# Kernel optimization log

Measured on AMD Instinct MI355X. Metric: run time of the kernel, lower is better.

Reference implementation:

```python
import jax, jax.numpy as jnp
import numpy as np

L1_PENALTY = 0.01
RHO = 5.0
N_ITERS = 100  # fixed iteration count standing in for max_iter=2000 w/ tol
EPS = 1e-12


def _normalize(x):
    # matches torch.nn.functional.normalize(dim=1, eps=1e-12)
    n = jnp.linalg.norm(x, axis=-1, keepdims=True)
    return x / jnp.maximum(n, EPS)


def _admm_nnlasso(D, Y, lam, rho, n_iters):
    """Batched nonnegative Lasso via ADMM.
    Solves per-row: min_w 0.5*||D^T w - y||^2 + lam*||w||_1, w >= 0.
    D: [c, d] dictionary, Y: [B, d] targets. Returns W: [B, c].
    x-update uses Woodbury: (A^T A + rho I)^{-1} b = (b - A^T (G + rho I)^{-1} A b)/rho
    with A = D^T, G = A A^T = D^T D ([d, d], d=512 -> cheap Cholesky).
    """
    d = D.shape[1]
    G = D.T @ D + rho * jnp.eye(d, dtype=D.dtype)  # [d, d]
    cf = jax.scipy.linalg.cho_factor(G)
    Aty = Y @ D.T  # [B, c] = A^T y batched
    thr = lam / rho

    def step(carry, _):
        z, u = carry
        b = Aty + rho * (z - u)               # [B, c]
        s = jax.scipy.linalg.cho_solve(cf, (b @ D).T).T  # [B, d]
        x = (b - s @ D.T) / rho               # [B, c]
        z_new = jnp.maximum(x + u - thr, 0.0)  # nonneg soft-threshold
        u_new = u + x - z_new
        return (z_new, u_new), None

    z0 = jnp.zeros_like(Aty)
    (z, _), _ = jax.lax.scan(step, (z0, z0), None, length=n_iters)
    return z


def setup_inputs() -> dict:
    key = jax.random.key(0)
    k1, k2, k3, k4 = jax.random.split(key, 4)
    B, C, Dm = 1024, 10000, 512
    image = jax.random.normal(k1, (B, Dm), dtype=jnp.float32)
    text = jax.random.normal(k2, (B, Dm), dtype=jnp.float32)
    image_mean = 0.1 * jax.random.normal(k3, (Dm,), dtype=jnp.float32)
    dictionary = jax.random.normal(k4, (C, Dm), dtype=jnp.float32)
    dictionary = dictionary / jnp.linalg.norm(dictionary, axis=1, keepdims=True)
    return {"image": image, "text": text, "image_mean": image_mean,
            "dictionary": dictionary}


def reference(image, text, image_mean, dictionary):
    # encode_image
    img = _normalize(image)
    centered = _normalize(img - image_mean)
    weights = _admm_nnlasso(dictionary, centered, L1_PENALTY, RHO, N_ITERS)
    recon = weights @ dictionary           # [B, d]
    recon = _normalize(recon)
    recon = _normalize(recon + image_mean)
    # encode_text (decomp_text=False -> just normalize)
    txt = _normalize(text)
    return recon, txt
```

## Files before the change

kernel.cpp:

```cpp
#include <hip/hip_runtime.h>
#include <cstddef>
#include <cstdint>

#define BDIM  1024
#define DM    512
#define CREAL 10000
#define CP    10112
#define KSPL  16
#define RHOC  5.0f
#define THRC  (0.01f/5.0f)
#define NIT   100
#define NSIT  12

typedef float f32x4 __attribute__((ext_vector_type(4)));
typedef _Float16 f16x8 __attribute__((ext_vector_type(8)));
typedef _Float16 f16x4 __attribute__((ext_vector_type(4)));
typedef unsigned int u32x4 __attribute__((ext_vector_type(4)));


__device__ __forceinline__ f16x8 scl6(f16x8 v) {
    f16x8 r;
#pragma unroll
    for (int i = 0; i < 8; i++) r[i] = v[i] * (_Float16)0.015625f;
    return r;
}

__device__ __forceinline__ void absfold(f16x8& h8, f16x8& l8) {
    u32x4 h = __builtin_bit_cast(u32x4, h8);
    u32x4 l = __builtin_bit_cast(u32x4, l8);
    u32x4 m = h & 0x80008000u;
    h8 = __builtin_bit_cast(f16x8, h ^ m);
    l8 = __builtin_bit_cast(f16x8, l ^ m);
}

__device__ __forceinline__ void relufold(f16x8& h8, f16x8& l8) {
#pragma unroll
    for (int e = 0; e < 8; e++) {
        bool p = h8[e] > (_Float16)0;
        if (!p) { h8[e] = (_Float16)0; l8[e] = (_Float16)0; }
    }
}

__device__ __forceinline__ size_t psidx(int row, int col) {
    return ((size_t)(row >> 4) * (CP >> 5) + (size_t)(col >> 5)) * 512
         + (size_t)((((col >> 3) & 3) * 16 + (row & 15)) * 8 + (col & 7));
}

__device__ __forceinline__ void dma16(const _Float16* g, _Float16* l) {
    __builtin_amdgcn_global_load_lds(
        (const __attribute__((address_space(1))) void*)g,
        (__attribute__((address_space(3))) void*)l, 16, 0, 0);
}

__device__ __forceinline__ float blk_sum256(float v) {
    __shared__ float sb[4];
#pragma unroll
    for (int o = 32; o; o >>= 1) v += __shfl_down(v, o, 64);
    int lane = threadIdx.x & 63, w = threadIdx.x >> 6;
    __syncthreads();
    if (lane == 0) sb[w] = v;
    __syncthreads();
    return sb[0] + sb[1] + sb[2] + sb[3];
}

__global__ __launch_bounds__(256) void knorm_rows(const float* __restrict__ X,
                                                  float* __restrict__ out) {
    int row = blockIdx.x, t = threadIdx.x;
    int off = row * DM + t * 2;
    float2 v = *(const float2*)(X + off);
    float ss = blk_sum256(v.x * v.x + v.y * v.y);
    float inv = 1.0f / fmaxf(sqrtf(ss), 1e-12f);
    float2 o = {v.x * inv, v.y * inv};
    *(float2*)(out + off) = o;
}

__global__ __launch_bounds__(256) void kprep_Y(const float* __restrict__ img,
                                               const float* __restrict__ mean,
                                               float* __restrict__ Y) {
    int row = blockIdx.x, t = threadIdx.x;
    int off = row * DM + t * 2;
    float2 v = *(const float2*)(img + off);
    float ss = blk_sum256(v.x * v.x + v.y * v.y);
    float inv = 1.0f / fmaxf(sqrtf(ss), 1e-12f);
    float2 mm = *(const float2*)(mean + t * 2);
    float tx = v.x * inv - mm.x, ty = v.y * inv - mm.y;
    float ss2 = blk_sum256(tx * tx + ty * ty);
    float inv2 = 1.0f / fmaxf(sqrtf(ss2), 1e-12f);
    float2 o = {tx * inv2, ty * inv2};
    *(float2*)(Y + off) = o;
}

__global__ __launch_bounds__(256) void ktrs(const float* __restrict__ in,
                                            float* __restrict__ out32,
                                            _Float16* __restrict__ oH,
                                            _Float16* __restrict__ oL,
                                            int Rvalid, int Cin, int Rout) {
    __shared__ float tile[64][65];
    int r0 = blockIdx.x * 64;
    int c0 = blockIdx.y * 64;
    int t = threadIdx.x;
    int ri = r0 + (t >> 2);
    int cc = (t & 3) * 16;
#pragma unroll
    for (int q = 0; q < 4; ++q) {
        float4 v = {0.f, 0.f, 0.f, 0.f};
        if (ri < Rvalid) v = *(const float4*)(in + (size_t)ri * Cin + c0 + cc + q * 4);
        *(float4*)&tile[t >> 2][cc + q * 4] = v;
    }
    __syncthreads();
    int oc = c0 + (t >> 2);
    int orr = r0 + (t & 3) * 16;
    _Float16 hv[16], lv[16];
#pragma unroll
    for (int q = 0; q < 16; ++q) {
        float v = tile[(t & 3) * 16 + q][t >> 2];
        _Float16 h = (_Float16)v;
        _Float16 l = (_Float16)((v - (float)h) * 64.f);
        hv[q] = h; lv[q] = l;
        if (out32) out32[(size_t)oc * Rout + orr + q] = (float)h + (float)l * 0.015625f;
    }
    int rt = oc >> 4, rin = oc & 15;
    int kt = orr >> 5;
    int kq0 = (orr >> 3) & 3;
    size_t base = ((size_t)rt * (Rout >> 5) + kt) * 512;
    *(f16x8*)(oH + base + (size_t)(kq0 * 16 + rin) * 8)       = *(f16x8*)&hv[0];
    *(f16x8*)(oH + base + (size_t)((kq0 + 1) * 16 + rin) * 8) = *(f16x8*)&hv[8];
    *(f16x8*)(oL + base + (size_t)(kq0 * 16 + rin) * 8)       = *(f16x8*)&lv[0];
    *(f16x8*)(oL + base + (size_t)((kq0 + 1) * 16 + rin) * 8) = *(f16x8*)&lv[8];
}

__global__ void kcsum(const float* __restrict__ Dt, float* __restrict__ csum) {
    int n = blockIdx.x, t = threadIdx.x;
    float s = 0.f;
    for (int k = t; k < CP; k += 64) s += Dt[(size_t)n * CP + k];
#pragma unroll
    for (int o = 32; o; o >>= 1) s += __shfl_down(s, o, 64);
    if (t == 0) csum[n] = s;
}

__global__ __launch_bounds__(256) void kG(const float* __restrict__ Dt,
                                          float* __restrict__ G) {
    __shared__ float As[32][68];
    __shared__ float Bs[32][68];
    int tid = threadIdx.x;
    int j0 = blockIdx.x * 64, i0 = blockIdx.y * 64;
    int tn = (tid & 15) * 4, tm = (tid >> 4) * 4;
    float acc[4][4];
#pragma unroll
    for (int i = 0; i < 4; i++)
#pragma unroll
        for (int j = 0; j < 4; j++) acc[i][j] = 0.f;
    for (int k0 = 0; k0 < CP; k0 += 32) {
        __syncthreads();
#pragma unroll
        for (int p = 0; p < 2; ++p) {
            int idx = tid + p * 256;
            int row = idx >> 3, kv = (idx & 7) << 2;
            float4 va = *(const float4*)(Dt + (size_t)(i0 + row) * CP + k0 + kv);
            As[kv + 0][row] = va.x; As[kv + 1][row] = va.y;
            As[kv + 2][row] = va.z; As[kv + 3][row] = va.w;
            float4 vb = *(const float4*)(Dt + (size_t)(j0 + row) * CP + k0 + kv);
            Bs[kv + 0][row] = vb.x; Bs[kv + 1][row] = vb.y;
            Bs[kv + 2][row] = vb.z; Bs[kv + 3][row] = vb.w;
        }
        __syncthreads();
#pragma unroll
        for (int k = 0; k < 32; ++k) {
            float4 a4 = *(const float4*)&As[k][tm];
            float4 b4 = *(const float4*)&Bs[k][tn];
            float af[4] = {a4.x, a4.y, a4.z, a4.w};
            float bf[4] = {b4.x, b4.y, b4.z, b4.w};
#pragma unroll
            for (int i = 0; i < 4; i++)
#pragma unroll
                for (int j = 0; j < 4; j++) acc[i][j] = fmaf(af[i], bf[j], acc[i][j]);
        }
    }
#pragma unroll
    for (int i = 0; i < 4; i++)
#pragma unroll
        for (int j = 0; j < 4; j++) {
            int gi = i0 + tm + i, gj = j0 + tn + j;
            G[gi * DM + gj] = acc[i][j] + ((gi == gj) ? RHOC : 0.f);
        }
}

__global__ void krow_abssum(const float* __restrict__ G, float* __restrict__ gmax) {
    int row = blockIdx.x, t = threadIdx.x;
    float s = 0.f;
    for (int j = t; j < DM; j += 64) s += fabsf(G[row * DM + j]);
#pragma unroll
    for (int o = 32; o; o >>= 1) s += __shfl_down(s, o, 64);
    if (t == 0) atomicMax((int*)gmax, __float_as_int(s));
}

__global__ void kinit_X0(const float* __restrict__ gmax, float* __restrict__ X) {
    int idx = blockIdx.x * 256 + threadIdx.x;
    int i = idx >> 9, j = idx & 511;
    X[idx] = (i == j) ? (1.0f / gmax[0]) : 0.0f;
}

__global__ __launch_bounds__(256) void kgemm_ns_T(const float* __restrict__ G,
                                                  const float* __restrict__ X,
                                                  float* __restrict__ T) {
    __shared__ float As[32][68];
    __shared__ float Bs[32][68];
    int tid = threadIdx.x;
    int n0 = blockIdx.x * 64, m0 = blockIdx.y * 64;
    int tn = (tid & 15) * 4, tm = (tid >> 4) * 4;
    float acc[4][4];
#pragma unroll
    for (int i = 0; i < 4; i++)
#pragma unroll
        for (int j = 0; j < 4; j++) acc[i][j] = 0.f;
    for (int k0 = 0; k0 < DM; k0 += 32) {
        __syncthreads();
#pragma unroll
        for (int p = 0; p < 2; ++p) {
            int idx = tid + p * 256;
            {
                int row = idx >> 3, kv = (idx & 7) << 2;
                float4 v = *(const float4*)(G + (m0 + row) * DM + k0 + kv);
                As[kv + 0][row] = v.x; As[kv + 1][row] = v.y;
                As[kv + 2][row] = v.z; As[kv + 3][row] = v.w;
            }
            {
                int r = idx >> 4, cv = (idx & 15) << 2;
                *(float4*)&Bs[r][cv] = *(const float4*)(X + (k0 + r) * DM + n0 + cv);
            }
        }
        __syncthreads();
#pragma unroll
        for (int k = 0; k < 32; ++k) {
            float4 a4 = *(const float4*)&As[k][tm];
            float4 b4 = *(const float4*)&Bs[k][tn];
            float af[4] = {a4.x, a4.y, a4.z, a4.w};
            float bf[4] = {b4.x, b4.y, b4.z, b4.w};
#pragma unroll
            for (int i = 0; i < 4; i++)
#pragma unroll
                for (int j = 0; j < 4; j++) acc[i][j] = fmaf(af[i], bf[j], acc[i][j]);
        }
    }
#pragma unroll
    for (int i = 0; i < 4; i++) {
        float4 o = {acc[i][0], acc[i][1], acc[i][2], acc[i][3]};
        *(float4*)(T + (m0 + tm + i) * DM + n0 + tn) = o;
    }
}

__global__ __launch_bounds__(256) void kgemm_ns_X(const float* __restrict__ Xo,
                                                  const float* __restrict__ T,
                                                  float* __restrict__ Xn) {
    __shared__ float As[32][68];
    __shared__ float Bs[32][68];
    int tid = threadIdx.x;
    int n0 = blockIdx.x * 64, m0 = blockIdx.y * 64;
    int tn = (tid & 15) * 4, tm = (tid >> 4) * 4;
    float acc[4][4];
#pragma unroll
    for (int i = 0; i < 4; i++)
#pragma unroll
        for (int j = 0; j < 4; j++) acc[i][j] = 0.f;
    for (int k0 = 0; k0 < DM; k0 += 32) {
        __syncthreads();
#pragma unroll
        for (int p = 0; p < 2; ++p) {
            int idx = tid + p * 256;
            {
                int row = idx >> 3, kv = (idx & 7) << 2;
                float4 v = *(const float4*)(Xo + (m0 + row) * DM + k0 + kv);
                As[kv + 0][row] = v.x; As[kv + 1][row] = v.y;
                As[kv + 2][row] = v.z; As[kv + 3][row] = v.w;
            }
            {
                int r = idx >> 4, cv = (idx & 15) << 2;
                *(float4*)&Bs[r][cv] = *(const float4*)(T + (k0 + r) * DM + n0 + cv);
            }
        }
        __syncthreads();
#pragma unroll
        for (int k = 0; k < 32; ++k) {
            float4 a4 = *(const float4*)&As[k][tm];
            float4 b4 = *(const float4*)&Bs[k][tn];
            float af[4] = {a4.x, a4.y, a4.z, a4.w};
            float bf[4] = {b4.x, b4.y, b4.z, b4.w};
#pragma unroll
            for (int i = 0; i < 4; i++)
#pragma unroll
                for (int j = 0; j < 4; j++) acc[i][j] = fmaf(af[i], bf[j], acc[i][j]);
        }
    }
#pragma unroll
    for (int i = 0; i < 4; i++) {
        int base = (m0 + tm + i) * DM + n0 + tn;
        float4 xo = *(const float4*)(Xo + base);
        float4 o = {2.f * xo.x - acc[i][0], 2.f * xo.y - acc[i][1],
                    2.f * xo.z - acc[i][2], 2.f * xo.w - acc[i][3]};
        *(float4*)(Xn + base) = o;
    }
}

template <int MODE>
__global__ __launch_bounds__(256) void kgemm_nn64(const float* __restrict__ A,
                                                  const float* __restrict__ B,
                                                  float* __restrict__ out32,
                                                  _Float16* __restrict__ oA) {
    __shared__ float As[32][68];
    __shared__ float Bs[32][68];
    int tid = threadIdx.x;
    int n0 = blockIdx.x * 64, m0 = blockIdx.y * 64;
    int tn = (tid & 15) * 4, tm = (tid >> 4) * 4;
    float acc[4][4];
#pragma unroll
    for (int i = 0; i < 4; i++)
#pragma unroll
        for (int j = 0; j < 4; j++) acc[i][j] = 0.f;
    for (int k0 = 0; k0 < DM; k0 += 32) {
        __syncthreads();
#pragma unroll
        for (int p = 0; p < 2; ++p) {
            int idx = tid + p * 256;
            {
                int row = idx >> 3, kv = (idx & 7) << 2;
                float4 v = *(const float4*)(A + (size_t)(m0 + row) * DM + k0 + kv);
                As[kv + 0][row] = v.x; As[kv + 1][row] = v.y;
                As[kv + 2][row] = v.z; As[kv + 3][row] = v.w;
            }
            {
                int r = idx >> 4, cv = (idx & 15) << 2;
                *(float4*)&Bs[r][cv] = *(const float4*)(B + (size_t)(k0 + r) * CP + n0 + cv);
            }
        }
        __syncthreads();
#pragma unroll
        for (int k = 0; k < 32; ++k) {
            float4 a4 = *(const float4*)&As[k][tm];
            float4 b4 = *(const float4*)&Bs[k][tn];
            float af[4] = {a4.x, a4.y, a4.z, a4.w};
            float bf[4] = {b4.x, b4.y, b4.z, b4.w};
#pragma unroll
            for (int i = 0; i < 4; i++)
#pragma unroll
                for (int j = 0; j < 4; j++) acc[i][j] = fmaf(af[i], bf[j], acc[i][j]);
        }
    }
#pragma unroll
    for (int i = 0; i < 4; i++)
#pragma unroll
        for (int j = 0; j < 4; j++) {
            int row = m0 + tm + i, col = n0 + tn + j;
            if (MODE == 0) out32[(size_t)row * CP + col] = acc[i][j];
            else           oA[psidx(row, col)] = (_Float16)(acc[i][j] * 0.2f * 64.f);
        }
}

__global__ __launch_bounds__(256) void kgemm_aD(const float* __restrict__ Yb,
                                                const float* __restrict__ G,
                                                const float* __restrict__ csum,
                                                float* __restrict__ aD) {
    __shared__ float As[32][68];
    __shared__ float Bs[32][68];
    int tid = threadIdx.x;
    int n0 = blockIdx.x * 64, m0 = blockIdx.y * 64;
    int tn = (tid & 15) * 4, tm = (tid >> 4) * 4;
    float acc[4][4];
#pragma unroll
    for (int i = 0; i < 4; i++)
#pragma unroll
        for (int j = 0; j < 4; j++) acc[i][j] = 0.f;
    for (int k0 = 0; k0 < DM; k0 += 32) {
        __syncthreads();
#pragma unroll
        for (int p = 0; p < 2; ++p) {
            int idx = tid + p * 256;
            {
                int row = idx >> 3, kv = (idx & 7) << 2;
                float4 v = *(const float4*)(Yb + (size_t)(m0 + row) * DM + k0 + kv);
                As[kv + 0][row] = v.x; As[kv + 1][row] = v.y;
                As[kv + 2][row] = v.z; As[kv + 3][row] = v.w;
            }
            {
                int r = idx >> 4, cv = (idx & 15) << 2;
                *(float4*)&Bs[r][cv] = *(const float4*)(G + (k0 + r) * DM + n0 + cv);
            }
        }
        __syncthreads();
#pragma unroll
        for (int k = 0; k < 32; ++k) {
            float4 a4 = *(const float4*)&As[k][tm];
            float4 b4 = *(const float4*)&Bs[k][tn];
            float af[4] = {a4.x, a4.y, a4.z, a4.w};
            float bf[4] = {b4.x, b4.y, b4.z, b4.w};
#pragma unroll
            for (int i = 0; i < 4; i++)
#pragma unroll
                for (int j = 0; j < 4; j++) acc[i][j] = fmaf(af[i], bf[j], acc[i][j]);
        }
    }
    float4 c4 = *(const float4*)(csum + n0 + tn);
#pragma unroll
    for (int i = 0; i < 4; i++) {
        int base = (m0 + tm + i) * DM + n0 + tn;
        float4 y4 = *(const float4*)(Yb + base);
        float4 o = {acc[i][0] * 0.2f - y4.x - THRC * c4.x,
                    acc[i][1] * 0.2f - y4.y - THRC * c4.y,
                    acc[i][2] * 0.2f - y4.z - THRC * c4.z,
                    acc[i][3] * 0.2f - y4.w - THRC * c4.w};
        *(float4*)(aD + base) = o;
    }
}

__global__ void kinit_s(_Float16* __restrict__ SHp, _Float16* __restrict__ SLp) {
    size_t i = ((size_t)blockIdx.x * 256 + threadIdx.x) * 8;
    _Float16 h = (_Float16)(-THRC);
    _Float16 l = (_Float16)((-THRC - (float)h) * 64.f);
    f16x8 hv, lv;
#pragma unroll
    for (int e = 0; e < 8; e++) { hv[e] = h; lv[e] = l; }
    *(f16x8*)(SHp + i) = hv;
    *(f16x8*)(SLp + i) = lv;
}


__device__ __forceinline__ void stage2(_Float16* __restrict__ sab,
                                       const _Float16* __restrict__ AHp,
                                       const _Float16* __restrict__ ALp,
                                       const _Float16* __restrict__ BHp,
                                       const _Float16* __restrict__ BLp,
                                       int sp, int mtbB, int ntbB, int ktA, int ktB,
                                       int wvu, int lane) {
#pragma unroll
    for (int k = 0; k < 4; ++k) {
        const int c = wvu * 4 + k;
        const int t = (c >> 1) & 7;
        const int p = c & 1;
        const _Float16* gp;
        if (c < 16) gp = (p ? ALp : AHp) + ((size_t)(mtbB + t) * ktA + sp) * 512 + (size_t)lane * 8;
        else        gp = (p ? BLp : BHp) + ((size_t)(ntbB + t) * ktB + sp) * 512 + (size_t)lane * 8;
        dma16(gp, sab + (size_t)c * 512);
    }
}

template <int FOLD>
__device__ __forceinline__ void compute8(const _Float16* __restrict__ sab,
                                         int wm, int wn, int lane,
                                         f32x4 (&acc)[4][2]) {
    const int ta = wm >> 4;
    const int tb = wn >> 4;
    f16x8 bh[2], bl[2], bs_[2];
#pragma unroll
    for (int j = 0; j < 2; ++j) {
        const _Float16* p = sab + 8192 + (size_t)(tb + j) * 1024 + (size_t)lane * 8;
        bh[j] = *(const f16x8*)p;
        bl[j] = *(const f16x8*)(p + 512);
        bs_[j] = scl6(bh[j]);
    }
    f16x8 ah[4], al[4], as_[4];
#pragma unroll
    for (int i = 0; i < 4; ++i) {
        const _Float16* p = sab + (size_t)(ta + i) * 1024 + (size_t)lane * 8;
        ah[i] = *(const f16x8*)p;
        al[i] = *(const f16x8*)(p + 512);
    }
#pragma unroll
    for (int i = 0; i < 4; ++i) {
        if (FOLD == 0) absfold(ah[i], al[i]);
        else if (FOLD == 1) relufold(ah[i], al[i]);
        as_[i] = scl6(ah[i]);
    }
    __builtin_amdgcn_s_setprio(1);
#pragma unroll
    for (int i = 0; i < 4; ++i)
#pragma unroll
        for (int j = 0; j < 2; ++j) {
            acc[i][j] = __builtin_amdgcn_mfma_f32_16x16x32_f16(ah[i],  bh[j], acc[i][j], 0, 0, 0);
            acc[i][j] = __builtin_amdgcn_mfma_f32_16x16x32_f16(as_[i], bl[j], acc[i][j], 0, 0, 0);
            acc[i][j] = __builtin_amdgcn_mfma_f32_16x16x32_f16(al[i],  bs_[j], acc[i][j], 0, 0, 0);
        }
    __builtin_amdgcn_s_setprio(0);
}

template <int MODE>
__global__ __launch_bounds__(512, 4) void kg1f(const _Float16* __restrict__ SHp,
                                               const _Float16* __restrict__ SLp,
                                               const _Float16* __restrict__ DHs,
                                               const _Float16* __restrict__ DLs,
                                               float* __restrict__ Qp) {
    __shared__ _Float16 sAB[2][16384];
    const int raw = blockIdx.x;
    const int xcd = raw & 7;
    const int r   = raw >> 3;
    const int ks  = xcd * 2 + (r & 1);
    const int q   = r >> 1;
    const int mb  = q >> 2, nb = q & 3;
    const int n0 = nb * 128, m0 = mb * 128;
    const int tid = threadIdx.x;
    const int lane = tid & 63;
    const int wvu = tid >> 6;
    const int wm = (wvu >> 2) * 64;
    const int wn = (wvu & 3) * 32;
    f32x4 acc[4][2] = {};

    const int steps = CP / 32;
    const int per = (steps + KSPL - 1) / KSPL;
    int s0 = ks * per;
    int s1 = s0 + per; if (s1 > steps) s1 = steps;

    const int mtbB = m0 >> 4;
    const int ntbB = n0 >> 4;
    const int KT = CP / 32;

    stage2(sAB[0], SHp, SLp, DHs, DLs, s0, mtbB, ntbB, KT, KT, wvu, lane);
    __syncthreads();

    for (int sp = s0; sp < s1; sp += 2) {
        stage2(sAB[1], SHp, SLp, DHs, DLs, sp + 1, mtbB, ntbB, KT, KT, wvu, lane);
        compute8<MODE>(sAB[0], wm, wn, lane, acc);
        __syncthreads();
        if (sp + 2 < s1)
            stage2(sAB[0], SHp, SLp, DHs, DLs, sp + 2, mtbB, ntbB, KT, KT, wvu, lane);
        compute8<MODE>(sAB[1], wm, wn, lane, acc);
        __syncthreads();
    }

    float* outp = Qp + (size_t)ks * (BDIM * DM);
    const int r0 = (lane >> 4) * 4, c0l = lane & 15;
#pragma unroll
    for (int i = 0; i < 4; i++)
#pragma unroll
        for (int v = 0; v < 4; v++) {
            int row = m0 + wm + i * 16 + r0 + v;
#pragma unroll
            for (int j = 0; j < 2; j++)
                outp[(size_t)row * DM + n0 + wn + j * 16 + c0l] = acc[i][j][v];
        }
}

template <int ADD>
__global__ void kredf(const float* __restrict__ Qp, const float* __restrict__ aD,
                      float* __restrict__ out32, _Float16* __restrict__ QH,
                      _Float16* __restrict__ QL) {
    size_t b = ((size_t)blockIdx.x * 256 + threadIdx.x) * 4;
    float4 s = {0.f, 0.f, 0.f, 0.f};
    if (ADD) s = *(const float4*)(aD + b);
#pragma unroll
    for (int qq = 0; qq < KSPL; qq++) {
        float4 t = *(const float4*)(Qp + (size_t)qq * (BDIM * DM) + b);
        s.x += t.x; s.y += t.y; s.z += t.z; s.w += t.w;
    }
    if (ADD) {
        int row = (int)(b >> 9), col = (int)(b & 511);
        size_t t0 = ((size_t)(row >> 4) * 16 + (size_t)(col >> 5)) * 512
                  + (size_t)((((col >> 3) & 3) * 16 + (row & 15)) * 8 + (col & 7));
        float sv[4] = {s.x, s.y, s.z, s.w};
        f16x4 h4, l4;
#pragma unroll
        for (int e = 0; e < 4; e++) {
            _Float16 h = (_Float16)sv[e];
            h4[e] = h;
            l4[e] = (_Float16)((sv[e] - (float)h) * 64.f);
        }
        *(f16x4*)(QH + t0) = h4;
        *(f16x4*)(QL + t0) = l4;
    } else {
        *(float4*)(out32 + b) = s;
    }
}

__global__ __launch_bounds__(512, 4) void kg2f(const _Float16* __restrict__ QH,
                                               const _Float16* __restrict__ QL,
                                               const _Float16* __restrict__ EHs,
                                               const _Float16* __restrict__ ELs,
                                               const _Float16* __restrict__ AH,
                                               _Float16* __restrict__ SHp,
                                               _Float16* __restrict__ SLp) {
    __shared__ _Float16 sAB[2][16384];
    const int raw = blockIdx.x;
    const int g = raw & 7;
    const int q = raw >> 3;
    const int mb = q & 7, jj = q >> 3;
    const int nb = g * 10 + jj;
    if (nb >= 79) return;
    const int n0 = nb * 128, m0 = mb * 128;
    const int tid = threadIdx.x;
    const int lane = tid & 63;
    const int wvu = tid >> 6;
    const int wm = (wvu >> 2) * 64;
    const int wn = (wvu & 3) * 32;
    const int mtbB = m0 >> 4;
    const int ntbB = n0 >> 4;
    const int KT = DM / 32;
    f32x4 acc[4][2] = {};

    stage2(sAB[0], QH, QL, EHs, ELs, 0, mtbB, ntbB, KT, KT, wvu, lane);
    __syncthreads();

    for (int kk = 0; kk < KT; kk += 2) {
        stage2(sAB[1], QH, QL, EHs, ELs, kk + 1, mtbB, ntbB, KT, KT, wvu, lane);
        compute8<2>(sAB[0], wm, wn, lane, acc);
        __syncthreads();
        if (kk + 2 < KT)
            stage2(sAB[0], QH, QL, EHs, ELs, kk + 2, mtbB, ntbB, KT, KT, wvu, lane);
        compute8<2>(sAB[1], wm, wn, lane, acc);
        __syncthreads();
    }

    const int r0 = (lane >> 4) * 4, c0l = lane & 15;
    const int mtbA = (m0 + wm) >> 4;
    const int ktb  = (n0 + wn) >> 5;
#pragma unroll
    for (int i = 0; i < 4; ++i) {
        float* sT = (float*)(&sAB[i & 1][0]) + wvu * (16 * 36);
#pragma unroll
        for (int j = 0; j < 2; ++j)
#pragma unroll
            for (int v = 0; v < 4; ++v)
                sT[(r0 + v) * 36 + j * 16 + c0l] = acc[i][j][v];
        float e[8];
        *(float4*)&e[0] = *(const float4*)&sT[(lane & 15) * 36 + (lane >> 4) * 8];
        *(float4*)&e[4] = *(const float4*)&sT[(lane & 15) * 36 + (lane >> 4) * 8 + 4];
        size_t base = ((size_t)(mtbA + i) * (CP >> 5) + ktb) * 512 + (size_t)lane * 8;
        f16x8 ah8 = *(const f16x8*)(AH + base);
        f16x8 sh8 = *(const f16x8*)(SHp + base);
        f16x8 sl8 = *(const f16x8*)(SLp + base);
        f16x8 nh, nl;
#pragma unroll
        for (int e8 = 0; e8 < 8; ++e8) {
            float a = (float)ah8[e8] * 0.015625f;
            float sold = (float)sh8[e8] + (float)sl8[e8] * 0.015625f;
            float z = fmaxf(sold, 0.f);
            float pn = a + z - e[e8];
            float sn = pn - THRC;
            _Float16 h = (_Float16)sn;
            nh[e8] = h;
            nl[e8] = (_Float16)((sn - (float)h) * 64.f);
        }
        *(f16x8*)(SHp + base) = nh;
        *(f16x8*)(SLp + base) = nl;
    }
}

__global__ __launch_bounds__(256) void kfinal(const float* __restrict__ Qf,
                                              const float* __restrict__ mean,
                                              float* __restrict__ out) {
    int row = blockIdx.x, t = threadIdx.x;
    int off = row * DM + t * 2;
    float2 qv = *(const float2*)(Qf + off);
    float rx = qv.x, ry = qv.y;
    float ss = blk_sum256(rx * rx + ry * ry);
    float inv = 1.0f / fmaxf(sqrtf(ss), 1e-12f);
    rx *= inv; ry *= inv;
    float2 mm = *(const float2*)(mean + t * 2);
    rx += mm.x; ry += mm.y;
    float ss2 = blk_sum256(rx * rx + ry * ry);
    float inv2 = 1.0f / fmaxf(sqrtf(ss2), 1e-12f);
    float2 o = {rx * inv2, ry * inv2};
    *(float2*)(out + off) = o;
}

extern "C" void kernel_launch(void* const* d_in, const int* in_sizes, int n_in,
                              void* d_out, int out_size, void* d_ws, size_t ws_size,
                              hipStream_t stream) {
    const float* image = (const float*)d_in[0];
    const float* text  = (const float*)d_in[1];
    const float* mean  = (const float*)d_in[2];
    const float* D     = (const float*)d_in[3];
    float* out = (float*)d_out;
    float* ws = (float*)d_ws;

    const size_t PLH = (size_t)DM * CP;
    float* aD   = ws;
    _Float16* QH = (_Float16*)(ws + 524288);
    _Float16* QL = QH + (size_t)BDIM * DM;
    _Float16* DHs = (_Float16*)(ws + 1048576);
    _Float16* DLs = DHs + PLH;
    _Float16* EHs = DLs + PLH;
    _Float16* ELs = EHs + PLH;
    _Float16* AH  = ELs + PLH;
    _Float16* SH  = AH + (size_t)BDIM * CP;
    _Float16* SL  = SH + (size_t)BDIM * CP;
    float* Qp   = (float*)(SL + (size_t)BDIM * CP);
    float* csum = Qp + (size_t)KSPL * BDIM * DM;
    float* gmax = csum + 512;
    float* Dt32 = (float*)SH;
    float* G    = Dt32 + (size_t)DM * CP;
    float* Xa   = G + 262144;
    float* Xb   = Xa + 262144;
    float* Tns  = Xb + 262144;
    float* Y    = Tns + 262144;
    float* Et32 = (float*)AH;

    knorm_rows<<<BDIM, 256, 0, stream>>>(text, out + (size_t)BDIM * DM);
    kprep_Y<<<BDIM, 256, 0, stream>>>(image, mean, Y);
    ktrs<<<dim3(CP / 64, DM / 64), 256, 0, stream>>>(D, Dt32, DHs, DLs, CREAL, DM, CP);
    kcsum<<<DM, 64, 0, stream>>>(Dt32, csum);
    kG<<<dim3(8, 8), 256, 0, stream>>>(Dt32, G);
    (void)hipMemsetAsync(gmax, 0, 4, stream);
    krow_abssum<<<DM, 64, 0, stream>>>(G, gmax);
    kinit_X0<<<DM * DM / 256, 256, 0, stream>>>(gmax, Xa);
    float* xc = Xa;
    float* xn = Xb;
    for (int it = 0; it < NSIT; ++it) {
        kgemm_ns_T<<<dim3(8, 8), 256, 0, stream>>>(G, xc, Tns);
        kgemm_ns_X<<<dim3(8, 8), 256, 0, stream>>>(xc, Tns, xn);
        float* tmp = xc; xc = xn; xn = tmp;
    }
    float* Ginv = xc;
    kgemm_nn64<0><<<dim3(CP / 64, DM / 64), 256, 0, stream>>>(Ginv, Dt32, Et32, nullptr);
    ktrs<<<dim3(DM / 64, CP / 64), 256, 0, stream>>>(Et32, nullptr, EHs, ELs, DM, CP, DM);
    kgemm_nn64<1><<<dim3(CP / 64, BDIM / 64), 256, 0, stream>>>(Y, Dt32, nullptr, AH);
    kgemm_aD<<<dim3(DM / 64, BDIM / 64), 256, 0, stream>>>(Y, G, csum, aD);
    kinit_s<<<(int)((size_t)BDIM * CP / 8 / 256), 256, 0, stream>>>(SH, SL);

    for (int it = 0; it < NIT; ++it) {
        kg1f<0><<<512, 512, 0, stream>>>(SH, SL, DHs, DLs, Qp);
        kredf<1><<<BDIM * DM / 1024, 256, 0, stream>>>(Qp, aD, nullptr, QH, QL);
        kg2f<<<640, 512, 0, stream>>>(QH, QL, EHs, ELs, AH, SH, SL);
    }

    kg1f<1><<<512, 512, 0, stream>>>(SH, SL, DHs, DLs, Qp);
    kredf<0><<<BDIM * DM / 1024, 256, 0, stream>>>(Qp, nullptr, aD, nullptr, nullptr);
    kfinal<<<BDIM, 256, 0, stream>>>(aD, mean, out);
}
```

Measured before the change: 9.524 ms.

## Retile kg2f to 64x128 blocks with 4 waves and dedicated staging

The second ADMM GEMM kernel now uses 64-row by 128-column output tiles with 256 threads (4 waves, each covering 64x32) instead of 128x128 tiles with 512 threads. It gets its own staging and compute helpers, and the grid doubles to 1280 blocks with an XCD-aware mapping. The aim is more blocks, better load balance across CUs and less LDS per block. In exchange, the E operand is reloaded more often because each block covers fewer rows.

```diff
diff --git a/kernel.cpp b/kernel.cpp
--- a/kernel.cpp
+++ b/kernel.cpp
@@ -568,46 +568,98 @@
     }
 }
 
-__global__ __launch_bounds__(512, 4) void kg2f(const _Float16* __restrict__ QH,
+__device__ __forceinline__ void stage_g2(_Float16* __restrict__ sab,
+                                         const _Float16* __restrict__ QHp,
+                                         const _Float16* __restrict__ QLp,
+                                         const _Float16* __restrict__ EHp,
+                                         const _Float16* __restrict__ ELp,
+                                         int sp, int mtbB, int ntbB,
+                                         int wvu, int lane) {
+#pragma unroll
+    for (int k = 0; k < 6; ++k) {
+        const int c = wvu * 6 + k;
+        const _Float16* gp;
+        if (c < 8) {
+            const int t = c >> 1, p = c & 1;
+            gp = (p ? QLp : QHp) + ((size_t)(mtbB + t) * 16 + sp) * 512 + (size_t)lane * 8;
+        } else {
+            const int cc = c - 8, t = cc >> 1, p = cc & 1;
+            gp = (p ? ELp : EHp) + ((size_t)(ntbB + t) * 16 + sp) * 512 + (size_t)lane * 8;
+        }
+        dma16(gp, sab + (size_t)c * 512);
+    }
+}
+
+__device__ __forceinline__ void compute4(const _Float16* __restrict__ sab,
+                                         int wn, int lane, f32x4 (&acc)[4][2]) {
+    const int tb = wn >> 4;
+    f16x8 bh[2], bl[2], bs_[2];
+#pragma unroll
+    for (int j = 0; j < 2; ++j) {
+        const _Float16* p = sab + 4096 + (size_t)(tb + j) * 1024 + (size_t)lane * 8;
+        bh[j] = *(const f16x8*)p;
+        bl[j] = *(const f16x8*)(p + 512);
+        bs_[j] = scl6(bh[j]);
+    }
+    f16x8 ah[4], al[4], as_[4];
+#pragma unroll
+    for (int i = 0; i < 4; ++i) {
+        const _Float16* p = sab + (size_t)i * 1024 + (size_t)lane * 8;
+        ah[i] = *(const f16x8*)p;
+        al[i] = *(const f16x8*)(p + 512);
+        as_[i] = scl6(ah[i]);
+    }
+    __builtin_amdgcn_s_setprio(1);
+#pragma unroll
+    for (int i = 0; i < 4; ++i)
+#pragma unroll
+        for (int j = 0; j < 2; ++j) {
+            acc[i][j] = __builtin_amdgcn_mfma_f32_16x16x32_f16(ah[i],  bh[j], acc[i][j], 0, 0, 0);
+            acc[i][j] = __builtin_amdgcn_mfma_f32_16x16x32_f16(as_[i], bl[j], acc[i][j], 0, 0, 0);
+            acc[i][j] = __builtin_amdgcn_mfma_f32_16x16x32_f16(al[i],  bs_[j], acc[i][j], 0, 0, 0);
+        }
+    __builtin_amdgcn_s_setprio(0);
+}
+
+__global__ __launch_bounds__(256, 3) void kg2f(const _Float16* __restrict__ QH,
                                                const _Float16* __restrict__ QL,
                                                const _Float16* __restrict__ EHs,
                                                const _Float16* __restrict__ ELs,
                                                const _Float16* __restrict__ AH,
                                                _Float16* __restrict__ SHp,
                                                _Float16* __restrict__ SLp) {
-    __shared__ _Float16 sAB[2][16384];
+    __shared__ _Float16 sAB[2][12288];
     const int raw = blockIdx.x;
-    const int g = raw & 7;
-    const int q = raw >> 3;
-    const int mb = q & 7, jj = q >> 3;
-    const int nb = g * 10 + jj;
+    const int xcd = raw & 7;
+    const int r = raw >> 3;
+    const int nb = xcd * 10 + (r >> 4);
+    const int mb = r & 15;
     if (nb >= 79) return;
-    const int n0 = nb * 128, m0 = mb * 128;
+    const int n0 = nb * 128, m0 = mb * 64;
     const int tid = threadIdx.x;
     const int lane = tid & 63;
     const int wvu = tid >> 6;
-    const int wm = (wvu >> 2) * 64;
-    const int wn = (wvu & 3) * 32;
+    const int wn = wvu * 32;
     const int mtbB = m0 >> 4;
     const int ntbB = n0 >> 4;
     const int KT = DM / 32;
     f32x4 acc[4][2] = {};
 
-    stage2(sAB[0], QH, QL, EHs, ELs, 0, mtbB, ntbB, KT, KT, wvu, lane);
+    stage_g2(sAB[0], QH, QL, EHs, ELs, 0, mtbB, ntbB, wvu, lane);
     __syncthreads();
 
     for (int kk = 0; kk < KT; kk += 2) {
-        stage2(sAB[1], QH, QL, EHs, ELs, kk + 1, mtbB, ntbB, KT, KT, wvu, lane);
-        compute8<2>(sAB[0], wm, wn, lane, acc);
+        stage_g2(sAB[1], QH, QL, EHs, ELs, kk + 1, mtbB, ntbB, wvu, lane);
+        compute4(sAB[0], wn, lane, acc);
         __syncthreads();
         if (kk + 2 < KT)
-            stage2(sAB[0], QH, QL, EHs, ELs, kk + 2, mtbB, ntbB, KT, KT, wvu, lane);
-        compute8<2>(sAB[1], wm, wn, lane, acc);
+            stage_g2(sAB[0], QH, QL, EHs, ELs, kk + 2, mtbB, ntbB, wvu, lane);
+        compute4(sAB[1], wn, lane, acc);
         __syncthreads();
     }
 
     const int r0 = (lane >> 4) * 4, c0l = lane & 15;
-    const int mtbA = (m0 + wm) >> 4;
+    const int mtbA = m0 >> 4;
     const int ktb  = (n0 + wn) >> 5;
 #pragma unroll
     for (int i = 0; i < 4; ++i) {
@@ -716,7 +768,7 @@
     for (int it = 0; it < NIT; ++it) {
         kg1f<0><<<512, 512, 0, stream>>>(SH, SL, DHs, DLs, Qp);
         kredf<1><<<BDIM * DM / 1024, 256, 0, stream>>>(Qp, aD, nullptr, QH, QL);
-        kg2f<<<640, 512, 0, stream>>>(QH, QL, EHs, ELs, AH, SH, SL);
+        kg2f<<<8 * 160, 256, 0, stream>>>(QH, QL, EHs, ELs, AH, SH, SL);
     }
 
     kg1f<1><<<512, 512, 0, stream>>>(SH, SL, DHs, DLs, Qp);
```

New measurement: 9.788 ms. +2.8%, slower.

## Fuse split-K reduction into kg1f via per-tile atomic counter barrier

Applied to the files above, without the earlier changes.

The separate split-K reduction kernel is removed from the ADMM loop. Each kg1f block now signals a per-output-tile atomic counter, spins until all 16 K-split blocks of that tile have written their partials, then reduces its slice of rows, adds aD, and writes the hi/lo fp16 split. This saves one kernel launch and a full pass over the partial buffer per iteration. In exchange it relies on all blocks of a tile being co-resident (512 blocks at 4 per CU) to avoid deadlock, uses spin-waiting, and writes scalar rather than vectorised fp16 stores.

```diff
diff --git a/kernel.cpp b/kernel.cpp
--- a/kernel.cpp
+++ b/kernel.cpp
@@ -481,12 +481,17 @@
     __builtin_amdgcn_s_setprio(0);
 }
 
-template <int MODE>
+template <int MODE, int FUSE>
 __global__ __launch_bounds__(512, 4) void kg1f(const _Float16* __restrict__ SHp,
                                                const _Float16* __restrict__ SLp,
                                                const _Float16* __restrict__ DHs,
                                                const _Float16* __restrict__ DLs,
-                                               float* __restrict__ Qp) {
+                                               float* __restrict__ Qp,
+                                               const float* __restrict__ aD,
+                                               _Float16* __restrict__ QH,
+                                               _Float16* __restrict__ QL,
+                                               unsigned* __restrict__ cnt,
+                                               unsigned target) {
     __shared__ _Float16 sAB[2][16384];
     const int raw = blockIdx.x;
     const int xcd = raw & 7;
@@ -535,37 +540,50 @@
             for (int j = 0; j < 2; j++)
                 outp[(size_t)row * DM + n0 + wn + j * 16 + c0l] = acc[i][j][v];
         }
-}
-
-template <int ADD>
-__global__ void kredf(const float* __restrict__ Qp, const float* __restrict__ aD,
-                      float* __restrict__ out32, _Float16* __restrict__ QH,
-                      _Float16* __restrict__ QL) {
+
+    if (FUSE) {
+        __threadfence();
+        __syncthreads();
+        const int tileId = mb * 4 + nb;
+        if (tid == 0) {
+            atomicAdd(&cnt[tileId], 1u);
+            while (atomicAdd(&cnt[tileId], 0u) < target) { }
+        }
+        __syncthreads();
+        __threadfence();
+        const int lr = tid >> 6;
+        const int lc = (tid & 63) * 2;
+        const int grow = m0 + ks * 8 + lr;
+        const int gcol = n0 + lc;
+        size_t off = (size_t)grow * DM + gcol;
+        float2 s2 = *(const float2*)(aD + off);
+#pragma unroll
+        for (int qq = 0; qq < KSPL; qq++) {
+            float2 t2 = *(const float2*)(Qp + (size_t)qq * (BDIM * DM) + off);
+            s2.x += t2.x; s2.y += t2.y;
+        }
+#pragma unroll
+        for (int e = 0; e < 2; e++) {
+            float sv = e ? s2.y : s2.x;
+            int col = gcol + e;
+            size_t t0 = ((size_t)(grow >> 4) * 16 + (size_t)(col >> 5)) * 512
+                      + (size_t)((((col >> 3) & 3) * 16 + (grow & 15)) * 8 + (col & 7));
+            _Float16 h = (_Float16)sv;
+            QH[t0] = h;
+            QL[t0] = (_Float16)((sv - (float)h) * 64.f);
+        }
+    }
+}
+
+__global__ void kredf0(const float* __restrict__ Qp, float* __restrict__ out32) {
     size_t b = ((size_t)blockIdx.x * 256 + threadIdx.x) * 4;
     float4 s = {0.f, 0.f, 0.f, 0.f};
-    if (ADD) s = *(const float4*)(aD + b);
 #pragma unroll
     for (int qq = 0; qq < KSPL; qq++) {
         float4 t = *(const float4*)(Qp + (size_t)qq * (BDIM * DM) + b);
         s.x += t.x; s.y += t.y; s.z += t.z; s.w += t.w;
     }
-    if (ADD) {
-        int row = (int)(b >> 9), col = (int)(b & 511);
-        size_t t0 = ((size_t)(row >> 4) * 16 + (size_t)(col >> 5)) * 512
-                  + (size_t)((((col >> 3) & 3) * 16 + (row & 15)) * 8 + (col & 7));
-        float sv[4] = {s.x, s.y, s.z, s.w};
-        f16x4 h4, l4;
-#pragma unroll
-        for (int e = 0; e < 4; e++) {
-            _Float16 h = (_Float16)sv[e];
-            h4[e] = h;
-            l4[e] = (_Float16)((sv[e] - (float)h) * 64.f);
-        }
-        *(f16x4*)(QH + t0) = h4;
-        *(f16x4*)(QL + t0) = l4;
-    } else {
-        *(float4*)(out32 + b) = s;
-    }
+    *(float4*)(out32 + b) = s;
 }
 
 __global__ __launch_bounds__(512, 4) void kg2f(const _Float16* __restrict__ QH,
@@ -683,6 +701,7 @@
     float* Qp   = (float*)(SL + (size_t)BDIM * CP);
     float* csum = Qp + (size_t)KSPL * BDIM * DM;
     float* gmax = csum + 512;
+    unsigned* cnt = (unsigned*)(gmax + 64);
     float* Dt32 = (float*)SH;
     float* G    = Dt32 + (size_t)DM * CP;
     float* Xa   = G + 262144;
@@ -697,6 +716,7 @@
     kcsum<<<DM, 64, 0, stream>>>(Dt32, csum);
     kG<<<dim3(8, 8), 256, 0, stream>>>(Dt32, G);
     (void)hipMemsetAsync(gmax, 0, 4, stream);
+    (void)hipMemsetAsync(cnt, 0, 32 * sizeof(unsigned), stream);
     krow_abssum<<<DM, 64, 0, stream>>>(G, gmax);
     kinit_X0<<<DM * DM / 256, 256, 0, stream>>>(gmax, Xa);
     float* xc = Xa;
@@ -714,12 +734,13 @@
     kinit_s<<<(int)((size_t)BDIM * CP / 8 / 256), 256, 0, stream>>>(SH, SL);
 
     for (int it = 0; it < NIT; ++it) {
-        kg1f<0><<<512, 512, 0, stream>>>(SH, SL, DHs, DLs, Qp);
-        kredf<1><<<BDIM * DM / 1024, 256, 0, stream>>>(Qp, aD, nullptr, QH, QL);
+        kg1f<0, 1><<<512, 512, 0, stream>>>(SH, SL, DHs, DLs, Qp, aD, QH, QL,
+                                            cnt, (unsigned)(16 * (it + 1)));
         kg2f<<<640, 512, 0, stream>>>(QH, QL, EHs, ELs, AH, SH, SL);
     }
 
-    kg1f<1><<<512, 512, 0, stream>>>(SH, SL, DHs, DLs, Qp);
-    kredf<0><<<BDIM * DM / 1024, 256, 0, stream>>>(Qp, nullptr, aD, nullptr, nullptr);
+    kg1f<1, 0><<<512, 512, 0, stream>>>(SH, SL, DHs, DLs, Qp,
+                                        nullptr, nullptr, nullptr, nullptr, 0u);
+    kredf0<<<BDIM * DM / 1024, 256, 0, stream>>>(Qp, aD);
     kfinal<<<BDIM, 256, 0, stream>>>(aD, mean, out);
 }
```

After: 33.61 ms. +252.9%, slower.
